# Kernel optimization log

Hardware: AMD Instinct MI355X
Metric: run time of the kernel (lower is better)

## Reference

```python
import jax, jax.numpy as jnp
import numpy as np

ALPHA = 0.5
B = 4096
K = 8192


def setup_inputs() -> dict:
    key = jax.random.key(0)
    k1, k2 = jax.random.split(key)
    outputs = jax.random.normal(k1, (B, K), dtype=jnp.float32)
    labels = jax.random.randint(k2, (B,), 0, K)
    targets = jax.nn.one_hot(labels, K, dtype=jnp.float32)
    S = jnp.eye(K, dtype=jnp.float32)          # soft-label matrix (state)
    S_t = jnp.zeros((K, K), dtype=jnp.float32)  # running stats (state)
    count = jnp.zeros((K, 1), dtype=jnp.float32)
    return {"outputs": outputs, "targets": targets, "S": S, "S_t": S_t, "count": count}


def reference(outputs, targets, S, S_t, count):
    # loss path
    ls = jax.nn.log_softmax(outputs, axis=1)          # [B, K]
    bsz = outputs.shape[0]
    target_label = jnp.argmax(targets, axis=1)        # [B]
    prediction = jnp.argmax(outputs, axis=1)          # [B]
    soft_targets = S[target_label]                    # [B, K] gather
    ce_hard = -(ls * targets).sum() / bsz
    ce_soft = -(ls * soft_targets).sum() / bsz
    loss = ALPHA * ce_hard + (1.0 - ALPHA) * ce_soft

    # stats accumulation (the original python for-loop, as one fused scatter-add)
    probs = jax.nn.softmax(jax.lax.stop_gradient(outputs), axis=1)  # [B, K]
    correct = (prediction == target_label).astype(probs.dtype)      # [B]
    S_t_new = S_t + jax.ops.segment_sum(probs * correct[:, None], target_label, num_segments=K)
    count_new = count + jax.ops.segment_sum(correct, target_label, num_segments=K)[:, None]
    return loss, S_t_new, count_new
```

## Files before the change

kernel.cpp:

```cpp
#include <hip/hip_runtime.h>
#include <math.h>

#define K 8192
#define BROWS 4096
#define ALPHA 0.5f

__device__ __forceinline__ void argmax_combine(float& v, int& i, float v2, int i2){
  if (v2 > v || (v2 == v && i2 < i)) { v = v2; i = i2; }
}

__global__ __launch_bounds__(256) void row_stats_kernel(
    const float* __restrict__ outputs,
    const float* __restrict__ targets,
    const float* __restrict__ S,
    float* __restrict__ rowloss,
    int*   __restrict__ rowtl,
    int*   __restrict__ rowcorrect,
    float* __restrict__ rowm,
    float* __restrict__ rowinvZ)
{
  const int b = blockIdx.x;
  const int t = threadIdx.x;
  const int lane = t & 63;
  const int wid  = t >> 6;

  const float4* orow = (const float4*)(outputs + (size_t)b * K);
  float x[32];
#pragma unroll
  for (int i = 0; i < 8; ++i){
    float4 v = orow[i*256 + t];
    x[4*i+0]=v.x; x[4*i+1]=v.y; x[4*i+2]=v.z; x[4*i+3]=v.w;
  }

  float mv = -INFINITY; int mi = 0x7fffffff;
#pragma unroll
  for (int i = 0; i < 8; ++i){
#pragma unroll
    for (int c = 0; c < 4; ++c){
      int idx = i*1024 + t*4 + c;
      argmax_combine(mv, mi, x[4*i+c], idx);
    }
  }

  const float4* trow = (const float4*)(targets + (size_t)b * K);
  float tv = -INFINITY; int ti = 0x7fffffff;
  float d_hard = 0.f, s_hard = 0.f;
#pragma unroll
  for (int i = 0; i < 8; ++i){
    float4 v = trow[i*256 + t];
    float tc[4] = {v.x, v.y, v.z, v.w};
#pragma unroll
    for (int c = 0; c < 4; ++c){
      int idx = i*1024 + t*4 + c;
      d_hard += x[4*i+c] * tc[c];
      s_hard += tc[c];
      argmax_combine(tv, ti, tc[c], idx);
    }
  }

#pragma unroll
  for (int off = 32; off; off >>= 1){
    float v2 = __shfl_down(mv, off, 64); int i2 = __shfl_down(mi, off, 64);
    argmax_combine(mv, mi, v2, i2);
    v2 = __shfl_down(tv, off, 64); i2 = __shfl_down(ti, off, 64);
    argmax_combine(tv, ti, v2, i2);
  }

  __shared__ float s_v[2][4]; __shared__ int s_i[2][4];
  __shared__ float s_m; __shared__ int s_pred; __shared__ int s_tl;
  if (lane == 0){ s_v[0][wid]=mv; s_i[0][wid]=mi; s_v[1][wid]=tv; s_i[1][wid]=ti; }
  __syncthreads();
  if (t == 0){
    float av=s_v[0][0]; int ai=s_i[0][0];
    float bv=s_v[1][0]; int bi=s_i[1][0];
#pragma unroll
    for (int w=1; w<4; ++w){
      argmax_combine(av, ai, s_v[0][w], s_i[0][w]);
      argmax_combine(bv, bi, s_v[1][w], s_i[1][w]);
    }
    s_m = av; s_pred = ai; s_tl = bi;
  }
  __syncthreads();
  const float m  = s_m;
  const int   tl = s_tl;

  float se = 0.f;
#pragma unroll
  for (int i = 0; i < 32; ++i) se += expf(x[i] - m);

  const float4* srow = (const float4*)(S + (size_t)tl * K);
  float d_soft = 0.f, s_soft = 0.f;
#pragma unroll
  for (int i = 0; i < 8; ++i){
    float4 v = srow[i*256 + t];
    d_soft += x[4*i+0]*v.x + x[4*i+1]*v.y + x[4*i+2]*v.z + x[4*i+3]*v.w;
    s_soft += v.x + v.y + v.z + v.w;
  }

  float sums[5] = {d_hard, s_hard, se, d_soft, s_soft};
#pragma unroll
  for (int off = 32; off; off >>= 1){
#pragma unroll
    for (int j = 0; j < 5; ++j) sums[j] += __shfl_down(sums[j], off, 64);
  }
  __shared__ float s_sums[4][5];
  if (lane == 0){
#pragma unroll
    for (int j = 0; j < 5; ++j) s_sums[wid][j] = sums[j];
  }
  __syncthreads();
  if (t == 0){
    float tot[5];
#pragma unroll
    for (int j=0;j<5;++j) tot[j] = s_sums[0][j]+s_sums[1][j]+s_sums[2][j]+s_sums[3][j];
    float Z = tot[2];
    float logZ = logf(Z);
    float ceh = -(tot[0] - (m + logZ) * tot[1]);
    float ces = -(tot[3] - (m + logZ) * tot[4]);
    rowloss[b]    = (ALPHA * ceh + (1.0f - ALPHA) * ces) * (1.0f / (float)BROWS);
    rowtl[b]      = tl;
    rowcorrect[b] = (s_pred == tl) ? 1 : 0;
    rowm[b]       = m;
    rowinvZ[b]    = 1.0f / Z;
  }
}

__global__ __launch_bounds__(256) void copy_st_kernel(const float* __restrict__ src,
                                                      float* __restrict__ dst){
  size_t base = (size_t)blockIdx.x * 8192 + threadIdx.x;
#pragma unroll
  for (int j = 0; j < 32; ++j)
    dst[base + (size_t)j*256] = src[base + (size_t)j*256];
}

__global__ __launch_bounds__(256) void loss_count_kernel(const float* __restrict__ rowloss,
                                                         const float* __restrict__ count,
                                                         float* __restrict__ out_loss,
                                                         float* __restrict__ out_count){
  int t = threadIdx.x;
  float s = 0.f;
  for (int i = t; i < BROWS; i += 256) s += rowloss[i];
#pragma unroll
  for (int off = 32; off; off >>= 1) s += __shfl_down(s, off, 64);
  __shared__ float sh[4];
  if ((t & 63) == 0) sh[t >> 6] = s;
  __syncthreads();
  if (t == 0) out_loss[0] = sh[0] + sh[1] + sh[2] + sh[3];
  for (int i = t; i < K; i += 256) out_count[i] = count[i];
}

__global__ __launch_bounds__(256) void scatter_kernel(const float* __restrict__ outputs,
    const int* __restrict__ rowtl, const int* __restrict__ rowcorrect,
    const float* __restrict__ rowm, const float* __restrict__ rowinvZ,
    float* __restrict__ out_St, float* __restrict__ out_count){
  int b = blockIdx.x;
  if (!rowcorrect[b]) return;
  int tl = rowtl[b];
  float m = rowm[b], invZ = rowinvZ[b];
  const float* orow = outputs + (size_t)b * K;
  float* drow = out_St + (size_t)tl * K;
  for (int k = threadIdx.x; k < K; k += 256)
    atomicAdd(&drow[k], expf(orow[k] - m) * invZ);
  if (threadIdx.x == 0) atomicAdd(&out_count[tl], 1.0f);
}

extern "C" void kernel_launch(void* const* d_in, const int* in_sizes, int n_in,
                              void* d_out, int out_size, void* d_ws, size_t ws_size,
                              hipStream_t stream) {
  const float* outputs = (const float*)d_in[0];
  const float* targets = (const float*)d_in[1];
  const float* S       = (const float*)d_in[2];
  const float* S_t     = (const float*)d_in[3];
  const float* count   = (const float*)d_in[4];

  float* out       = (float*)d_out;
  float* out_loss  = out;
  float* out_St    = out + 1;
  float* out_count = out + 1 + (size_t)K * K;

  float* rowloss    = (float*)d_ws;
  float* rowm       = rowloss + BROWS;
  float* rowinvZ    = rowm + BROWS;
  int*   rowtl      = (int*)(rowinvZ + BROWS);
  int*   rowcorrect = rowtl + BROWS;

  hipLaunchKernelGGL(row_stats_kernel, dim3(BROWS), dim3(256), 0, stream,
                     outputs, targets, S, rowloss, rowtl, rowcorrect, rowm, rowinvZ);
  hipLaunchKernelGGL(copy_st_kernel, dim3(8192), dim3(256), 0, stream, S_t, out_St);
  hipLaunchKernelGGL(loss_count_kernel, dim3(1), dim3(256), 0, stream,
                     rowloss, count, out_loss, out_count);
  hipLaunchKernelGGL(scatter_kernel, dim3(BROWS), dim3(256), 0, stream,
                     outputs, rowtl, rowcorrect, rowm, rowinvZ, out_St, out_count);
}
```

Measured before the change: 718.4 us.

## Vectorize aligned S_t copy, widen row-stats blocks, merge loss into scatter

The S_t copy now moves float4 stores aligned to the output offset (out+1 is misaligned by one float, so the destination is shifted by three), with unaligned vector loads from the source, a grid-stride loop and a scalar fix-up for the edge elements. The row statistics kernel moves to 512 threads per row, so each thread holds 16 values instead of 32. The single-block loss/count kernel is folded into the scatter launch as an extra block, removing one launch and its serialization. Risks: the unaligned source loads, and the scatter now being able to run on a block ordered relative to the count copy, which could race on out_count.

New measurement: 733.4 us. 2.1% more time.

```diff
diff --git a/kernel.cpp b/kernel.cpp
--- a/kernel.cpp
+++ b/kernel.cpp
@@ -5,11 +5,13 @@
 #define BROWS 4096
 #define ALPHA 0.5f
 
+typedef float f4u __attribute__((ext_vector_type(4), aligned(4)));
+
 __device__ __forceinline__ void argmax_combine(float& v, int& i, float v2, int i2){
   if (v2 > v || (v2 == v && i2 < i)) { v = v2; i = i2; }
 }
 
-__global__ __launch_bounds__(256) void row_stats_kernel(
+__global__ __launch_bounds__(512) void row_stats_kernel(
     const float* __restrict__ outputs,
     const float* __restrict__ targets,
     const float* __restrict__ S,
@@ -25,19 +27,19 @@
   const int wid  = t >> 6;
 
   const float4* orow = (const float4*)(outputs + (size_t)b * K);
-  float x[32];
-#pragma unroll
-  for (int i = 0; i < 8; ++i){
-    float4 v = orow[i*256 + t];
+  float x[16];
+#pragma unroll
+  for (int i = 0; i < 4; ++i){
+    float4 v = orow[i*512 + t];
     x[4*i+0]=v.x; x[4*i+1]=v.y; x[4*i+2]=v.z; x[4*i+3]=v.w;
   }
 
   float mv = -INFINITY; int mi = 0x7fffffff;
 #pragma unroll
-  for (int i = 0; i < 8; ++i){
+  for (int i = 0; i < 4; ++i){
 #pragma unroll
     for (int c = 0; c < 4; ++c){
-      int idx = i*1024 + t*4 + c;
+      int idx = i*2048 + t*4 + c;
       argmax_combine(mv, mi, x[4*i+c], idx);
     }
   }
@@ -46,12 +48,12 @@
   float tv = -INFINITY; int ti = 0x7fffffff;
   float d_hard = 0.f, s_hard = 0.f;
 #pragma unroll
-  for (int i = 0; i < 8; ++i){
-    float4 v = trow[i*256 + t];
+  for (int i = 0; i < 4; ++i){
+    float4 v = trow[i*512 + t];
     float tc[4] = {v.x, v.y, v.z, v.w};
 #pragma unroll
     for (int c = 0; c < 4; ++c){
-      int idx = i*1024 + t*4 + c;
+      int idx = i*2048 + t*4 + c;
       d_hard += x[4*i+c] * tc[c];
       s_hard += tc[c];
       argmax_combine(tv, ti, tc[c], idx);
@@ -66,7 +68,7 @@
     argmax_combine(tv, ti, v2, i2);
   }
 
-  __shared__ float s_v[2][4]; __shared__ int s_i[2][4];
+  __shared__ float s_v[2][8]; __shared__ int s_i[2][8];
   __shared__ float s_m; __shared__ int s_pred; __shared__ int s_tl;
   if (lane == 0){ s_v[0][wid]=mv; s_i[0][wid]=mi; s_v[1][wid]=tv; s_i[1][wid]=ti; }
   __syncthreads();
@@ -74,7 +76,7 @@
     float av=s_v[0][0]; int ai=s_i[0][0];
     float bv=s_v[1][0]; int bi=s_i[1][0];
 #pragma unroll
-    for (int w=1; w<4; ++w){
+    for (int w=1; w<8; ++w){
       argmax_combine(av, ai, s_v[0][w], s_i[0][w]);
       argmax_combine(bv, bi, s_v[1][w], s_i[1][w]);
     }
@@ -86,13 +88,13 @@
 
   float se = 0.f;
 #pragma unroll
-  for (int i = 0; i < 32; ++i) se += expf(x[i] - m);
+  for (int i = 0; i < 16; ++i) se += expf(x[i] - m);
 
   const float4* srow = (const float4*)(S + (size_t)tl * K);
   float d_soft = 0.f, s_soft = 0.f;
 #pragma unroll
-  for (int i = 0; i < 8; ++i){
-    float4 v = srow[i*256 + t];
+  for (int i = 0; i < 4; ++i){
+    float4 v = srow[i*512 + t];
     d_soft += x[4*i+0]*v.x + x[4*i+1]*v.y + x[4*i+2]*v.z + x[4*i+3]*v.w;
     s_soft += v.x + v.y + v.z + v.w;
   }
@@ -103,7 +105,7 @@
 #pragma unroll
     for (int j = 0; j < 5; ++j) sums[j] += __shfl_down(sums[j], off, 64);
   }
-  __shared__ float s_sums[4][5];
+  __shared__ float s_sums[8][5];
   if (lane == 0){
 #pragma unroll
     for (int j = 0; j < 5; ++j) s_sums[wid][j] = sums[j];
@@ -112,7 +114,12 @@
   if (t == 0){
     float tot[5];
 #pragma unroll
-    for (int j=0;j<5;++j) tot[j] = s_sums[0][j]+s_sums[1][j]+s_sums[2][j]+s_sums[3][j];
+    for (int j=0;j<5;++j){
+      float a = 0.f;
+#pragma unroll
+      for (int w=0;w<8;++w) a += s_sums[w][j];
+      tot[j] = a;
+    }
     float Z = tot[2];
     float logZ = logf(Z);
     float ceh = -(tot[0] - (m + logZ) * tot[1]);
@@ -127,41 +134,49 @@
 
 __global__ __launch_bounds__(256) void copy_st_kernel(const float* __restrict__ src,
                                                       float* __restrict__ dst){
-  size_t base = (size_t)blockIdx.x * 8192 + threadIdx.x;
-#pragma unroll
-  for (int j = 0; j < 32; ++j)
-    dst[base + (size_t)j*256] = src[base + (size_t)j*256];
-}
-
-__global__ __launch_bounds__(256) void loss_count_kernel(const float* __restrict__ rowloss,
-                                                         const float* __restrict__ count,
-                                                         float* __restrict__ out_loss,
-                                                         float* __restrict__ out_count){
-  int t = threadIdx.x;
-  float s = 0.f;
-  for (int i = t; i < BROWS; i += 256) s += rowloss[i];
-#pragma unroll
-  for (int off = 32; off; off >>= 1) s += __shfl_down(s, off, 64);
-  __shared__ float sh[4];
-  if ((t & 63) == 0) sh[t >> 6] = s;
-  __syncthreads();
-  if (t == 0) out_loss[0] = sh[0] + sh[1] + sh[2] + sh[3];
-  for (int i = t; i < K; i += 256) out_count[i] = count[i];
-}
-
-__global__ __launch_bounds__(256) void scatter_kernel(const float* __restrict__ outputs,
+  const f4u*  s4 = (const f4u*)(src + 3);
+  float4*     d4 = (float4*)(dst + 3);
+  const size_t n4 = 16777215UL;
+  size_t i = (size_t)blockIdx.x * blockDim.x + threadIdx.x;
+  const size_t stride = (size_t)gridDim.x * blockDim.x;
+  for (size_t j = i; j < n4; j += stride){
+    f4u v = s4[j];
+    d4[j] = *(const float4*)&v;
+  }
+  if (blockIdx.x == 0 && threadIdx.x < 4){
+    int idx = (threadIdx.x < 3) ? (int)threadIdx.x : 67108863;
+    dst[idx] = src[idx];
+  }
+}
+
+__global__ __launch_bounds__(256) void tail_kernel(const float* __restrict__ outputs,
     const int* __restrict__ rowtl, const int* __restrict__ rowcorrect,
     const float* __restrict__ rowm, const float* __restrict__ rowinvZ,
-    float* __restrict__ out_St, float* __restrict__ out_count){
-  int b = blockIdx.x;
+    const float* __restrict__ rowloss, const float* __restrict__ count,
+    float* __restrict__ out_loss, float* __restrict__ out_St,
+    float* __restrict__ out_count){
+  const int b = blockIdx.x;
+  const int t = threadIdx.x;
+  if (b == BROWS){
+    float s = 0.f;
+    for (int i = t; i < BROWS; i += 256) s += rowloss[i];
+#pragma unroll
+    for (int off = 32; off; off >>= 1) s += __shfl_down(s, off, 64);
+    __shared__ float sh[4];
+    if ((t & 63) == 0) sh[t >> 6] = s;
+    __syncthreads();
+    if (t == 0) out_loss[0] = sh[0] + sh[1] + sh[2] + sh[3];
+    for (int i = t; i < K; i += 256) out_count[i] = count[i];
+    return;
+  }
   if (!rowcorrect[b]) return;
-  int tl = rowtl[b];
-  float m = rowm[b], invZ = rowinvZ[b];
+  const int tl = rowtl[b];
+  const float m = rowm[b], invZ = rowinvZ[b];
   const float* orow = outputs + (size_t)b * K;
   float* drow = out_St + (size_t)tl * K;
-  for (int k = threadIdx.x; k < K; k += 256)
+  for (int k = t; k < K; k += 256)
     atomicAdd(&drow[k], expf(orow[k] - m) * invZ);
-  if (threadIdx.x == 0) atomicAdd(&out_count[tl], 1.0f);
+  if (t == 0) atomicAdd(&out_count[tl], 1.0f);
 }
 
 extern "C" void kernel_launch(void* const* d_in, const int* in_sizes, int n_in,
@@ -184,11 +199,10 @@
   int*   rowtl      = (int*)(rowinvZ + BROWS);
   int*   rowcorrect = rowtl + BROWS;
 
-  hipLaunchKernelGGL(row_stats_kernel, dim3(BROWS), dim3(256), 0, stream,
+  hipLaunchKernelGGL(row_stats_kernel, dim3(BROWS), dim3(512), 0, stream,
                      outputs, targets, S, rowloss, rowtl, rowcorrect, rowm, rowinvZ);
   hipLaunchKernelGGL(copy_st_kernel, dim3(8192), dim3(256), 0, stream, S_t, out_St);
-  hipLaunchKernelGGL(loss_count_kernel, dim3(1), dim3(256), 0, stream,
-                     rowloss, count, out_loss, out_count);
-  hipLaunchKernelGGL(scatter_kernel, dim3(BROWS), dim3(256), 0, stream,
-                     outputs, rowtl, rowcorrect, rowm, rowinvZ, out_St, out_count);
-}
+  hipLaunchKernelGGL(tail_kernel, dim3(BROWS + 1), dim3(256), 0, stream,
+                     outputs, rowtl, rowcorrect, rowm, rowinvZ, rowloss, count,
+                     out_loss, out_St, out_count);
+}
```

## Fuse S_t copy into row-stats grid and merge loss reduce into scatter

Applied to the files above, without the earlier changes.

The S_t-to-output copy is interleaved with the row-statistics work in one launch, with 2 of every 3 blocks copying rows. This lets the 256MB copy overlap with the row reductions. The loss/count reduction becomes an extra block of the scatter kernel, cutting four launches to two. The risk is that the extra block copies count while scatter blocks atomically add into out_count, so increments can be overwritten (a race), and that mixing block types may unbalance the grid.

Result: no change. 727.1 us (+1.2%).

```diff
diff --git a/kernel.cpp b/kernel.cpp
--- a/kernel.cpp
+++ b/kernel.cpp
@@ -9,18 +9,32 @@
   if (v2 > v || (v2 == v && i2 < i)) { v = v2; i = i2; }
 }
 
-__global__ __launch_bounds__(256) void row_stats_kernel(
+__global__ __launch_bounds__(256) void fused_kernel(
     const float* __restrict__ outputs,
     const float* __restrict__ targets,
     const float* __restrict__ S,
+    const float* __restrict__ S_t,
+    float* __restrict__ out_St,
     float* __restrict__ rowloss,
     int*   __restrict__ rowtl,
     int*   __restrict__ rowcorrect,
     float* __restrict__ rowm,
     float* __restrict__ rowinvZ)
 {
-  const int b = blockIdx.x;
-  const int t = threadIdx.x;
+  const int bb = blockIdx.x;
+  const int t  = threadIdx.x;
+  const int r  = bb % 3;
+
+  if (r != 0){
+    const int c = (bb / 3) * 2 + (r - 1);
+    size_t base = (size_t)c * 8192 + t;
+#pragma unroll
+    for (int j = 0; j < 32; ++j)
+      out_St[base + (size_t)j*256] = S_t[base + (size_t)j*256];
+    return;
+  }
+
+  const int b = bb / 3;
   const int lane = t & 63;
   const int wid  = t >> 6;
 
@@ -112,7 +126,8 @@
   if (t == 0){
     float tot[5];
 #pragma unroll
-    for (int j=0;j<5;++j) tot[j] = s_sums[0][j]+s_sums[1][j]+s_sums[2][j]+s_sums[3][j];
+    for (int j=0;j<5;++j)
+      tot[j] = s_sums[0][j]+s_sums[1][j]+s_sums[2][j]+s_sums[3][j];
     float Z = tot[2];
     float logZ = logf(Z);
     float ceh = -(tot[0] - (m + logZ) * tot[1]);
@@ -125,43 +140,34 @@
   }
 }
 
-__global__ __launch_bounds__(256) void copy_st_kernel(const float* __restrict__ src,
-                                                      float* __restrict__ dst){
-  size_t base = (size_t)blockIdx.x * 8192 + threadIdx.x;
-#pragma unroll
-  for (int j = 0; j < 32; ++j)
-    dst[base + (size_t)j*256] = src[base + (size_t)j*256];
-}
-
-__global__ __launch_bounds__(256) void loss_count_kernel(const float* __restrict__ rowloss,
-                                                         const float* __restrict__ count,
-                                                         float* __restrict__ out_loss,
-                                                         float* __restrict__ out_count){
-  int t = threadIdx.x;
-  float s = 0.f;
-  for (int i = t; i < BROWS; i += 256) s += rowloss[i];
-#pragma unroll
-  for (int off = 32; off; off >>= 1) s += __shfl_down(s, off, 64);
-  __shared__ float sh[4];
-  if ((t & 63) == 0) sh[t >> 6] = s;
-  __syncthreads();
-  if (t == 0) out_loss[0] = sh[0] + sh[1] + sh[2] + sh[3];
-  for (int i = t; i < K; i += 256) out_count[i] = count[i];
-}
-
-__global__ __launch_bounds__(256) void scatter_kernel(const float* __restrict__ outputs,
+__global__ __launch_bounds__(256) void tail_kernel(const float* __restrict__ outputs,
     const int* __restrict__ rowtl, const int* __restrict__ rowcorrect,
     const float* __restrict__ rowm, const float* __restrict__ rowinvZ,
-    float* __restrict__ out_St, float* __restrict__ out_count){
-  int b = blockIdx.x;
+    const float* __restrict__ rowloss, const float* __restrict__ count,
+    float* __restrict__ out_loss, float* __restrict__ out_St,
+    float* __restrict__ out_count){
+  const int b = blockIdx.x;
+  const int t = threadIdx.x;
+  if (b == BROWS){
+    float s = 0.f;
+    for (int i = t; i < BROWS; i += 256) s += rowloss[i];
+#pragma unroll
+    for (int off = 32; off; off >>= 1) s += __shfl_down(s, off, 64);
+    __shared__ float sh[4];
+    if ((t & 63) == 0) sh[t >> 6] = s;
+    __syncthreads();
+    if (t == 0) out_loss[0] = sh[0] + sh[1] + sh[2] + sh[3];
+    for (int i = t; i < K; i += 256) out_count[i] = count[i];
+    return;
+  }
   if (!rowcorrect[b]) return;
-  int tl = rowtl[b];
-  float m = rowm[b], invZ = rowinvZ[b];
+  const int tl = rowtl[b];
+  const float m = rowm[b], invZ = rowinvZ[b];
   const float* orow = outputs + (size_t)b * K;
   float* drow = out_St + (size_t)tl * K;
-  for (int k = threadIdx.x; k < K; k += 256)
+  for (int k = t; k < K; k += 256)
     atomicAdd(&drow[k], expf(orow[k] - m) * invZ);
-  if (threadIdx.x == 0) atomicAdd(&out_count[tl], 1.0f);
+  if (t == 0) atomicAdd(&out_count[tl], 1.0f);
 }
 
 extern "C" void kernel_launch(void* const* d_in, const int* in_sizes, int n_in,
@@ -184,11 +190,10 @@
   int*   rowtl      = (int*)(rowinvZ + BROWS);
   int*   rowcorrect = rowtl + BROWS;
 
-  hipLaunchKernelGGL(row_stats_kernel, dim3(BROWS), dim3(256), 0, stream,
-                     outputs, targets, S, rowloss, rowtl, rowcorrect, rowm, rowinvZ);
-  hipLaunchKernelGGL(copy_st_kernel, dim3(8192), dim3(256), 0, stream, S_t, out_St);
-  hipLaunchKernelGGL(loss_count_kernel, dim3(1), dim3(256), 0, stream,
-                     rowloss, count, out_loss, out_count);
-  hipLaunchKernelGGL(scatter_kernel, dim3(BROWS), dim3(256), 0, stream,
-                     outputs, rowtl, rowcorrect, rowm, rowinvZ, out_St, out_count);
+  hipLaunchKernelGGL(fused_kernel, dim3(3 * BROWS), dim3(256), 0, stream,
+                     outputs, targets, S, S_t, out_St,
+                     rowloss, rowtl, rowcorrect, rowm, rowinvZ);
+  hipLaunchKernelGGL(tail_kernel, dim3(BROWS + 1), dim3(256), 0, stream,
+                     outputs, rowtl, rowcorrect, rowm, rowinvZ, rowloss, count,
+                     out_loss, out_St, out_count);
 }
```
